# Optimization experiments

Hardware: AMD Instinct MI355X
Metric: run time of the kernel (lower is better)

The kernel has to match this reference:

```python
import jax, jax.numpy as jnp
import numpy as np

QMIN, QMAX = -128, 127

def make_accurate_lut():
    # lut[i, j] = signed8(j) * signed8(i) with indices taken as uint8 bit patterns
    v = np.arange(256)
    v[v >= 128] -= 256
    xx, yy = np.meshgrid(v, v)
    return jnp.asarray((xx * yy).astype(np.int32))

def setup_inputs() -> dict:
    key = jax.random.key(0)
    kx, kw = jax.random.split(key)
    B, N, M, K = 4, 512, 512, 256
    x = jax.random.normal(kx, (B, N, M), dtype=jnp.float32)
    w = jax.random.normal(kw, (K, M), dtype=jnp.float32)
    return {
        "x": x,
        "w": w,
        "lut": make_accurate_lut(),                       # [256,256] int32
        "x_scale": jnp.ones((1,), jnp.float32) * 0.03,    # per-tensor affine quant params
        "x_zero_point": jnp.zeros((1,), jnp.float32),
        "w_scale": jnp.ones((1,), jnp.float32) * 0.03,
        "w_zero_point": jnp.zeros((1,), jnp.float32),
    }

def _quantize(t, scale, zp):
    # affine quantize to signed int8 range, kept in int32 for indexing
    q = jnp.round(t / scale + zp)
    return jnp.clip(q, QMIN, QMAX).astype(jnp.int32)

def _lut_gemm(xq, wq, lut):
    # xq: [B,N,M] int32 in [-128,127]; wq: [K,M]; lut: [256,256]
    xi = jnp.mod(xq, 256)  # uint8 bit-pattern index
    wi = jnp.mod(wq, 256)
    # gather per-element products via the LUT, then accumulate over M
    prods = lut[xi[:, :, None, :], wi[None, None, :, :]]  # [B,N,K,M] int32
    return prods.sum(axis=-1)                             # [B,N,K] int32

def reference(x, w, lut, x_scale, x_zero_point, w_scale, w_zero_point):
    xs, xzp = x_scale.reshape(()), x_zero_point.reshape(())
    ws, wzp = w_scale.reshape(()), w_zero_point.reshape(())
    M = x.shape[-1]
    xq = _quantize(x, xs, xzp)           # [B,N,M]
    wq = _quantize(w, ws, wzp)           # [K,M]
    acc = _lut_gemm(xq, wq, lut).astype(jnp.float32)  # ~ sum_m xq*wq via LUT
    # affine zero-point correction: sum (xq-xzp)(wq-wzp)
    acc = (acc
           - wzp * jnp.sum(xq, axis=-1, keepdims=True).astype(jnp.float32)
           - xzp * jnp.sum(wq, axis=-1).astype(jnp.float32)[None, None, :]
           + jnp.float32(M) * xzp * wzp)
    return acc * xs * ws                 # dequantized output [B,N,K]
```

## Files before the change

### kernel.cpp

```cpp
#include <hip/hip_runtime.h>

constexpr int Mdim = 512;
constexpr int Kdim = 256;
constexpr int ROWS = 2048;
constexpr int MW   = Mdim / 4;

constexpr int XQ_OFF   = 0;
constexpr int WQ_OFF   = ROWS * MW;
constexpr int XSUM_OFF = WQ_OFF + Kdim * MW;
constexpr int WSUM_OFF = XSUM_OFF + ROWS;

typedef int v4i __attribute__((ext_vector_type(4)));

__device__ __forceinline__ int qz(float v, float scale, float zp) {
    float q = rintf(v / scale + zp);
    q = fminf(fmaxf(q, -128.0f), 127.0f);
    return (int)q;
}

__device__ __forceinline__ int pack4(int q0, int q1, int q2, int q3) {
    return (q0 & 255) | ((q1 & 255) << 8) | ((q2 & 255) << 16) | ((q3 & 255) << 24);
}

__global__ __launch_bounds__(64) void quant_kernel(
        const float* __restrict__ x, const float* __restrict__ w,
        const float* __restrict__ x_scale, const float* __restrict__ x_zp,
        const float* __restrict__ w_scale, const float* __restrict__ w_zp,
        int* __restrict__ ws) {
    const int tid = threadIdx.x;
    const bool is_x = (blockIdx.x < ROWS);
    const int row = is_x ? blockIdx.x : (blockIdx.x - ROWS);
    const float s  = is_x ? x_scale[0] : w_scale[0];
    const float zp = is_x ? x_zp[0]    : w_zp[0];
    const float* src = (is_x ? x : w) + (size_t)row * Mdim;

    const float4* src4 = (const float4*)src;
    float4 a = src4[tid * 2];
    float4 b = src4[tid * 2 + 1];

    int q0 = qz(a.x, s, zp), q1 = qz(a.y, s, zp), q2 = qz(a.z, s, zp), q3 = qz(a.w, s, zp);
    int q4 = qz(b.x, s, zp), q5 = qz(b.y, s, zp), q6 = qz(b.z, s, zp), q7 = qz(b.w, s, zp);

    const int base = (is_x ? XQ_OFF : WQ_OFF) + row * MW + 2 * tid;
    *(int2*)&ws[base] = make_int2(pack4(q0, q1, q2, q3), pack4(q4, q5, q6, q7));

    int sum = q0 + q1 + q2 + q3 + q4 + q5 + q6 + q7;
    #pragma unroll
    for (int off = 32; off > 0; off >>= 1) sum += __shfl_down(sum, off);
    if (tid == 0) ws[(is_x ? XSUM_OFF : WSUM_OFF) + row] = sum;
}

__global__ __launch_bounds__(64) void mfma_gemm_kernel(
        const int* __restrict__ ws,
        const float* __restrict__ x_scale, const float* __restrict__ x_zp,
        const float* __restrict__ w_scale, const float* __restrict__ w_zp,
        float* __restrict__ out) {
    const int lane  = threadIdx.x;
    const int group = lane >> 4;
    const int lo    = lane & 15;
    const int r0 = (blockIdx.x >> 3) * 16;
    const int c0 = (blockIdx.x & 7) * 32;

    const v4i* xa  = (const v4i*)&ws[XQ_OFF + (size_t)(r0 + lo) * MW];
    const v4i* wb0 = (const v4i*)&ws[WQ_OFF + (size_t)(c0 + lo) * MW];
    const v4i* wb1 = (const v4i*)&ws[WQ_OFF + (size_t)(c0 + 16 + lo) * MW];

    v4i a[8], b0[8], b1[8];
    #pragma unroll
    for (int kk = 0; kk < 8; ++kk) {
        a[kk]  = xa[kk * 4 + group];
        b0[kk] = wb0[kk * 4 + group];
        b1[kk] = wb1[kk * 4 + group];
    }

    v4i acc0 = {0, 0, 0, 0};
    v4i acc1 = {0, 0, 0, 0};
    #pragma unroll
    for (int kk = 0; kk < 8; ++kk) {
        acc0 = __builtin_amdgcn_mfma_i32_16x16x64_i8(a[kk], b0[kk], acc0, 0, 0, 0);
        acc1 = __builtin_amdgcn_mfma_i32_16x16x64_i8(a[kk], b1[kk], acc1, 0, 0, 0);
    }

    const float xs = x_scale[0], xzpf = x_zp[0];
    const float wsf = w_scale[0], wzpf = w_zp[0];
    const float oscale = xs * wsf;
    const float base_corr = (float)Mdim * xzpf * wzpf;
    const float wsum0 = (float)ws[WSUM_OFF + c0 + lo];
    const float wsum1 = (float)ws[WSUM_OFF + c0 + 16 + lo];
    const float corr0 = base_corr - xzpf * wsum0;
    const float corr1 = base_corr - xzpf * wsum1;
    const v4i xs4 = *(const v4i*)&ws[XSUM_OFF + r0 + group * 4];

    #pragma unroll
    for (int i = 0; i < 4; ++i) {
        const int row = r0 + group * 4 + i;
        const float xc = wzpf * (float)xs4[i];
        float v0 = (float)acc0[i] - xc + corr0;
        float v1 = (float)acc1[i] - xc + corr1;
        out[(size_t)row * Kdim + c0 + lo]      = v0 * oscale;
        out[(size_t)row * Kdim + c0 + 16 + lo] = v1 * oscale;
    }
}

extern "C" void kernel_launch(void* const* d_in, const int* in_sizes, int n_in,
                              void* d_out, int out_size, void* d_ws, size_t ws_size,
                              hipStream_t stream) {
    const float* x       = (const float*)d_in[0];
    const float* w       = (const float*)d_in[1];
    const float* x_scale = (const float*)d_in[3];
    const float* x_zp    = (const float*)d_in[4];
    const float* w_scale = (const float*)d_in[5];
    const float* w_zp    = (const float*)d_in[6];
    float* out = (float*)d_out;
    int* ws = (int*)d_ws;

    quant_kernel<<<ROWS + Kdim, 64, 0, stream>>>(x, w, x_scale, x_zp, w_scale, w_zp, ws);
    mfma_gemm_kernel<<<(ROWS / 16) * (Kdim / 32), 64, 0, stream>>>(
        ws, x_scale, x_zp, w_scale, w_zp, out);
}
```

Before: 72.00 us.

## Fuse quantization into MFMA GEMM and compute row sums with ones-MFMA

```diff
diff --git a/kernel.cpp b/kernel.cpp
--- a/kernel.cpp
+++ b/kernel.cpp
@@ -3,12 +3,6 @@
 constexpr int Mdim = 512;
 constexpr int Kdim = 256;
 constexpr int ROWS = 2048;
-constexpr int MW   = Mdim / 4;
-
-constexpr int XQ_OFF   = 0;
-constexpr int WQ_OFF   = ROWS * MW;
-constexpr int XSUM_OFF = WQ_OFF + Kdim * MW;
-constexpr int WSUM_OFF = XSUM_OFF + ROWS;
 
 typedef int v4i __attribute__((ext_vector_type(4)));
 
@@ -18,40 +12,14 @@
     return (int)q;
 }
 
-__device__ __forceinline__ int pack4(int q0, int q1, int q2, int q3) {
+__device__ __forceinline__ int qp4(float4 f, float s, float zp) {
+    int q0 = qz(f.x, s, zp), q1 = qz(f.y, s, zp);
+    int q2 = qz(f.z, s, zp), q3 = qz(f.w, s, zp);
     return (q0 & 255) | ((q1 & 255) << 8) | ((q2 & 255) << 16) | ((q3 & 255) << 24);
 }
 
-__global__ __launch_bounds__(64) void quant_kernel(
+__global__ __launch_bounds__(64) void fused_lutgemm_kernel(
         const float* __restrict__ x, const float* __restrict__ w,
-        const float* __restrict__ x_scale, const float* __restrict__ x_zp,
-        const float* __restrict__ w_scale, const float* __restrict__ w_zp,
-        int* __restrict__ ws) {
-    const int tid = threadIdx.x;
-    const bool is_x = (blockIdx.x < ROWS);
-    const int row = is_x ? blockIdx.x : (blockIdx.x - ROWS);
-    const float s  = is_x ? x_scale[0] : w_scale[0];
-    const float zp = is_x ? x_zp[0]    : w_zp[0];
-    const float* src = (is_x ? x : w) + (size_t)row * Mdim;
-
-    const float4* src4 = (const float4*)src;
-    float4 a = src4[tid * 2];
-    float4 b = src4[tid * 2 + 1];
-
-    int q0 = qz(a.x, s, zp), q1 = qz(a.y, s, zp), q2 = qz(a.z, s, zp), q3 = qz(a.w, s, zp);
-    int q4 = qz(b.x, s, zp), q5 = qz(b.y, s, zp), q6 = qz(b.z, s, zp), q7 = qz(b.w, s, zp);
-
-    const int base = (is_x ? XQ_OFF : WQ_OFF) + row * MW + 2 * tid;
-    *(int2*)&ws[base] = make_int2(pack4(q0, q1, q2, q3), pack4(q4, q5, q6, q7));
-
-    int sum = q0 + q1 + q2 + q3 + q4 + q5 + q6 + q7;
-    #pragma unroll
-    for (int off = 32; off > 0; off >>= 1) sum += __shfl_down(sum, off);
-    if (tid == 0) ws[(is_x ? XSUM_OFF : WSUM_OFF) + row] = sum;
-}
-
-__global__ __launch_bounds__(64) void mfma_gemm_kernel(
-        const int* __restrict__ ws,
         const float* __restrict__ x_scale, const float* __restrict__ x_zp,
         const float* __restrict__ w_scale, const float* __restrict__ w_zp,
         float* __restrict__ out) {
@@ -61,40 +29,54 @@
     const int r0 = (blockIdx.x >> 3) * 16;
     const int c0 = (blockIdx.x & 7) * 32;
 
-    const v4i* xa  = (const v4i*)&ws[XQ_OFF + (size_t)(r0 + lo) * MW];
-    const v4i* wb0 = (const v4i*)&ws[WQ_OFF + (size_t)(c0 + lo) * MW];
-    const v4i* wb1 = (const v4i*)&ws[WQ_OFF + (size_t)(c0 + 16 + lo) * MW];
+    const float xs   = x_scale[0], xzpf = x_zp[0];
+    const float wsf  = w_scale[0], wzpf = w_zp[0];
+
+    const float4* xr  = (const float4*)(x + (size_t)(r0 + lo) * Mdim) + group * 4;
+    const float4* wr0 = (const float4*)(w + (size_t)(c0 + lo) * Mdim) + group * 4;
+    const float4* wr1 = (const float4*)(w + (size_t)(c0 + 16 + lo) * Mdim) + group * 4;
 
     v4i a[8], b0[8], b1[8];
     #pragma unroll
     for (int kk = 0; kk < 8; ++kk) {
-        a[kk]  = xa[kk * 4 + group];
-        b0[kk] = wb0[kk * 4 + group];
-        b1[kk] = wb1[kk * 4 + group];
+        float4 f0 = xr[kk * 16 + 0], f1 = xr[kk * 16 + 1];
+        float4 f2 = xr[kk * 16 + 2], f3 = xr[kk * 16 + 3];
+        float4 g0 = wr0[kk * 16 + 0], g1 = wr0[kk * 16 + 1];
+        float4 g2 = wr0[kk * 16 + 2], g3 = wr0[kk * 16 + 3];
+        float4 h0 = wr1[kk * 16 + 0], h1 = wr1[kk * 16 + 1];
+        float4 h2 = wr1[kk * 16 + 2], h3 = wr1[kk * 16 + 3];
+        a[kk]  = (v4i){ qp4(f0, xs, xzpf),  qp4(f1, xs, xzpf),
+                        qp4(f2, xs, xzpf),  qp4(f3, xs, xzpf) };
+        b0[kk] = (v4i){ qp4(g0, wsf, wzpf), qp4(g1, wsf, wzpf),
+                        qp4(g2, wsf, wzpf), qp4(g3, wsf, wzpf) };
+        b1[kk] = (v4i){ qp4(h0, wsf, wzpf), qp4(h1, wsf, wzpf),
+                        qp4(h2, wsf, wzpf), qp4(h3, wsf, wzpf) };
     }
 
-    v4i acc0 = {0, 0, 0, 0};
-    v4i acc1 = {0, 0, 0, 0};
+    const v4i ones = {0x01010101, 0x01010101, 0x01010101, 0x01010101};
+    v4i acc0  = {0, 0, 0, 0};
+    v4i acc1  = {0, 0, 0, 0};
+    v4i accxs = {0, 0, 0, 0};
+    v4i accw0 = {0, 0, 0, 0};
+    v4i accw1 = {0, 0, 0, 0};
     #pragma unroll
     for (int kk = 0; kk < 8; ++kk) {
-        acc0 = __builtin_amdgcn_mfma_i32_16x16x64_i8(a[kk], b0[kk], acc0, 0, 0, 0);
-        acc1 = __builtin_amdgcn_mfma_i32_16x16x64_i8(a[kk], b1[kk], acc1, 0, 0, 0);
+        acc0  = __builtin_amdgcn_mfma_i32_16x16x64_i8(a[kk], b0[kk], acc0, 0, 0, 0);
+        acc1  = __builtin_amdgcn_mfma_i32_16x16x64_i8(a[kk], b1[kk], acc1, 0, 0, 0);
+        accxs = __builtin_amdgcn_mfma_i32_16x16x64_i8(a[kk], ones,   accxs, 0, 0, 0);
+        accw0 = __builtin_amdgcn_mfma_i32_16x16x64_i8(ones,  b0[kk], accw0, 0, 0, 0);
+        accw1 = __builtin_amdgcn_mfma_i32_16x16x64_i8(ones,  b1[kk], accw1, 0, 0, 0);
     }
 
-    const float xs = x_scale[0], xzpf = x_zp[0];
-    const float wsf = w_scale[0], wzpf = w_zp[0];
-    const float oscale = xs * wsf;
+    const float oscale    = xs * wsf;
     const float base_corr = (float)Mdim * xzpf * wzpf;
-    const float wsum0 = (float)ws[WSUM_OFF + c0 + lo];
-    const float wsum1 = (float)ws[WSUM_OFF + c0 + 16 + lo];
-    const float corr0 = base_corr - xzpf * wsum0;
-    const float corr1 = base_corr - xzpf * wsum1;
-    const v4i xs4 = *(const v4i*)&ws[XSUM_OFF + r0 + group * 4];
+    const float corr0 = base_corr - xzpf * (float)accw0[0];
+    const float corr1 = base_corr - xzpf * (float)accw1[0];
 
     #pragma unroll
     for (int i = 0; i < 4; ++i) {
         const int row = r0 + group * 4 + i;
-        const float xc = wzpf * (float)xs4[i];
+        const float xc = wzpf * (float)accxs[i];
         float v0 = (float)acc0[i] - xc + corr0;
         float v1 = (float)acc1[i] - xc + corr1;
         out[(size_t)row * Kdim + c0 + lo]      = v0 * oscale;
@@ -112,9 +94,8 @@
     const float* w_scale = (const float*)d_in[5];
     const float* w_zp    = (const float*)d_in[6];
     float* out = (float*)d_out;
-    int* ws = (int*)d_ws;
+    (void)d_ws; (void)ws_size;
 
-    quant_kernel<<<ROWS + Kdim, 64, 0, stream>>>(x, w, x_scale, x_zp, w_scale, w_zp, ws);
-    mfma_gemm_kernel<<<(ROWS / 16) * (Kdim / 32), 64, 0, stream>>>(
-        ws, x_scale, x_zp, w_scale, w_zp, out);
+    fused_lutgemm_kernel<<<(ROWS / 16) * (Kdim / 32), 64, 0, stream>>>(
+        x, w, x_scale, x_zp, w_scale, w_zp, out);
 }
```

New measurement: 82.11 us. +14.0%, slower.
